# Kernel optimization log

Measured on AMD Instinct MI355X. Metric: run time of the kernel, lower is better.

The kernel has to match this reference:

```python
import jax, jax.numpy as jnp
import numpy as np

N_NODES = 100000
N_EDGES = 3200000
D_FEAT = 512
D_HID = 64
D_LAT = 16
N_CLASS = 10
N_FLOW = 10
K_PROP = 10
ALPHA_TELEPORT = 0.1


def setup_inputs() -> dict:
    key = jax.random.key(0)
    ks = jax.random.split(key, 8)
    x = jax.random.normal(ks[0], (N_NODES, D_FEAT), jnp.float32)
    edge_index = jax.random.randint(ks[1], (2, N_EDGES), 0, N_NODES)
    p_c = jax.random.uniform(ks[2], (N_CLASS,), jnp.float32) + 0.1
    p_c = p_c / p_c.sum()
    W1 = jax.random.normal(ks[3], (D_FEAT, D_HID), jnp.float32) / np.sqrt(D_FEAT).astype(np.float32)
    b1 = jnp.zeros((D_HID,), jnp.float32)
    W2 = jax.random.normal(ks[4], (D_HID, D_LAT), jnp.float32) / np.sqrt(D_HID).astype(np.float32)
    b2 = jnp.zeros((D_LAT,), jnp.float32)
    flow_z0 = jax.random.normal(ks[5], (N_FLOW, N_CLASS, D_LAT), jnp.float32) * 0.1
    flow_alpha_prime = jax.random.normal(ks[6], (N_FLOW, N_CLASS, 1), jnp.float32) * 0.1
    flow_beta = jax.random.normal(ks[7], (N_FLOW, N_CLASS, 1), jnp.float32) * 0.1
    return dict(x=x, edge_index=edge_index, p_c=p_c, W1=W1, b1=b1, W2=W2, b2=b2,
                flow_z0=flow_z0, flow_alpha_prime=flow_alpha_prime, flow_beta=flow_beta)


def _batched_radial_log_prob(z, flow_z0, flow_alpha_prime, flow_beta):
    # Per-class batched radial flow (invertible pyro-style parameterization).
    # z: [N, D] -> log_q: [N, C]
    C, D = flow_z0.shape[1], flow_z0.shape[2]
    zz = jnp.broadcast_to(z[None], (C, z.shape[0], D))  # [C, N, D]
    sum_logdet = jnp.zeros((C, z.shape[0]), z.dtype)
    for l in range(flow_z0.shape[0]):  # small fixed number of flow layers
        z0 = flow_z0[l][:, None, :]                               # [C,1,D]
        alpha = jax.nn.softplus(flow_alpha_prime[l])[:, None, :]  # [C,1,1]
        beta_hat = -alpha + jax.nn.softplus(flow_beta[l])[:, None, :]
        dz = zz - z0
        r = jnp.sqrt(jnp.sum(dz * dz, axis=-1, keepdims=True))    # [C,N,1]
        h = 1.0 / (alpha + r)
        bh = beta_hat * h
        zz = zz + bh * dz
        logdet = (D - 1) * jnp.log1p(bh) + jnp.log1p(bh - beta_hat * r * h * h)
        sum_logdet = sum_logdet + logdet[..., 0]
    log_base = -0.5 * jnp.sum(zz * zz, axis=-1) - 0.5 * D * jnp.log(2.0 * jnp.pi)
    return (log_base + sum_logdet).T  # [N, C]


def _appnp(beta_ft, edge_index, n_nodes):
    # APPNP with self loops and symmetric gcn normalization over edge list.
    src = jnp.concatenate([edge_index[0], jnp.arange(n_nodes)])
    dst = jnp.concatenate([edge_index[1], jnp.arange(n_nodes)])
    deg = jax.ops.segment_sum(jnp.ones_like(src, dtype=beta_ft.dtype), dst, num_segments=n_nodes)
    dinv = jnp.where(deg > 0, jax.lax.rsqrt(jnp.maximum(deg, 1.0)), 0.0)
    norm = (dinv[src] * dinv[dst])[:, None]  # [E+N, 1]
    x0 = beta_ft
    b = beta_ft
    for _ in range(K_PROP):
        agg = jax.ops.segment_sum(norm * b[src], dst, num_segments=n_nodes)
        b = (1.0 - ALPHA_TELEPORT) * agg + ALPHA_TELEPORT * x0
    return b


def reference(x, edge_index, p_c, W1, b1, W2, b2, flow_z0, flow_alpha_prime, flow_beta):
    h = jax.nn.relu(x @ W1 + b1)           # input_encoder (dropout inactive at eval)
    z = h @ W2 + b2                        # latent_encoder, [N, D_LAT]
    log_q = _batched_radial_log_prob(z, flow_z0, flow_alpha_prime, flow_beta)
    log_q_per_class = log_q + jnp.log(p_c)[None, :]
    log_scale = 0.5 * D_LAT * jnp.log(4.0 * jnp.pi)  # 'latent-new' evidence scale
    beta_ft = jnp.exp(jnp.clip(log_q_per_class + log_scale, -30.0, 30.0))
    beta = _appnp(beta_ft, edge_index, x.shape[0])
    alpha = 1.0 + beta
    soft = alpha / jnp.sum(alpha, axis=-1, keepdims=True)
    hard = jnp.argmax(soft, axis=-1)
    return hard[:, None], soft
```

## Files before the change

kernel.cpp:

```cpp
#include <hip/hip_runtime.h>
#include <math.h>
#include <limits.h>

#define DF 512
#define DH 64
#define DL 16
#define NC 10
#define NF 10
#define KPROP 10

#define BSH 7
#define BW  (1 << BSH)
#define MAXB 1024
#define TILE 16384

__device__ __forceinline__ float softplus_(float x){
  return fmaxf(x, 0.0f) + log1pf(expf(-fabsf(x)));
}

#define BM 64
#define BN 64
#define BK 32
__global__ __launch_bounds__(256) void k_gemm1z(const float* __restrict__ x,
    const float* __restrict__ W1, const float* __restrict__ b1,
    const float* __restrict__ W2, const float* __restrict__ b2,
    float* __restrict__ z, int N)
{
  __shared__ float smem[2*BK*(BM+4)];
  float (*At)[BM+4] = (float(*)[BM+4])smem;
  float (*Bs)[BN+4] = (float(*)[BN+4])(smem + BK*(BM+4));
  __shared__ float W2s[DH][DL];
  __shared__ float b2s[DL];
  const int tid = threadIdx.x;
  for (int i = tid; i < DH*DL; i += 256) W2s[i>>4][i&15] = W2[i];
  if (tid < DL) b2s[tid] = b2[tid];
  const int tx = tid & 15, ty = tid >> 4;
  const int row0 = blockIdx.x * BM;
  float acc[4][4] = {};
  for (int k0 = 0; k0 < DF; k0 += BK) {
    #pragma unroll
    for (int i = 0; i < 2; ++i) {
      int idx = tid + i*256;
      int r  = idx >> 3;
      int kk = (idx & 7) << 2;
      int row = row0 + r;
      float4 va = make_float4(0.f,0.f,0.f,0.f);
      if (row < N) va = *(const float4*)&x[(size_t)row*DF + k0 + kk];
      At[kk+0][r]=va.x; At[kk+1][r]=va.y; At[kk+2][r]=va.z; At[kk+3][r]=va.w;
      int r2 = idx >> 4;
      int c4 = (idx & 15) << 2;
      float4 vb = *(const float4*)&W1[(size_t)(k0+r2)*DH + c4];
      Bs[r2][c4+0]=vb.x; Bs[r2][c4+1]=vb.y; Bs[r2][c4+2]=vb.z; Bs[r2][c4+3]=vb.w;
    }
    __syncthreads();
    #pragma unroll
    for (int kk = 0; kk < BK; ++kk) {
      float4 av = *(const float4*)&At[kk][ty<<2];
      float4 bv = *(const float4*)&Bs[kk][tx<<2];
      float a4[4]={av.x,av.y,av.z,av.w};
      float b4[4]={bv.x,bv.y,bv.z,bv.w};
      #pragma unroll
      for (int i=0;i<4;++i)
        #pragma unroll
        for (int j=0;j<4;++j) acc[i][j] = fmaf(a4[i], b4[j], acc[i][j]);
    }
    __syncthreads();
  }
  float4 bias = ((const float4*)b1)[tx];
  float bias4[4] = {bias.x, bias.y, bias.z, bias.w};
  float (*hs)[BM+4] = (float(*)[BM+4])smem;
  #pragma unroll
  for (int i=0;i<4;++i){
    #pragma unroll
    for (int j=0;j<4;++j)
      hs[(ty<<2)+i][(tx<<2)+j] = fmaxf(acc[i][j] + bias4[j], 0.0f);
  }
  __syncthreads();
  int row = tid >> 2, lg = tid & 3;
  float4 zacc = ((const float4*)b2s)[lg];
  #pragma unroll 8
  for (int k = 0; k < DH; ++k){
    float hv = hs[row][k];
    float4 wv = *(const float4*)&W2s[k][lg<<2];
    zacc.x = fmaf(hv, wv.x, zacc.x);
    zacc.y = fmaf(hv, wv.y, zacc.y);
    zacc.z = fmaf(hv, wv.z, zacc.z);
    zacc.w = fmaf(hv, wv.w, zacc.w);
  }
  int grow = row0 + row;
  if (grow < N) ((float4*)z)[(size_t)grow*4 + lg] = zacc;
}

__global__ __launch_bounds__(256) void k_flow2(const float* __restrict__ z,
    const float* __restrict__ pc, const float* __restrict__ z0g,
    const float* __restrict__ apg, const float* __restrict__ fbg,
    const float* __restrict__ dinv,
    float* __restrict__ x0, float* __restrict__ c0, float* __restrict__ y0, int N)
{
  __shared__ float z0s[NF][NC][DL];
  __shared__ float alps[NF][NC];
  __shared__ float bhs[NF][NC];
  __shared__ float lpc[NC];
  int tid = threadIdx.x;
  for (int i = tid; i < NF*NC*DL; i += 256)
    z0s[(i>>4)/NC][(i>>4)%NC][i&15] = z0g[i];
  if (tid < NF*NC){
    int l = tid/NC, c = tid%NC;
    float al = softplus_(apg[tid]);
    alps[l][c] = al;
    bhs[l][c]  = -al + softplus_(fbg[tid]);
  }
  if (tid < NC) lpc[tid] = __logf(pc[tid]);
  __syncthreads();

  int idx = blockIdx.x*256 + tid;
  int n = idx >> 4, c = idx & 15;
  if (n >= N) return;
  float dn = dinv[n];
  if (c >= NC){ x0[idx] = 0.f; c0[idx] = 0.f; y0[idx] = 0.f; return; }

  float zz[DL];
  const float4* z4 = (const float4*)z;
  #pragma unroll
  for (int q=0; q<4; ++q){
    float4 v = z4[(size_t)n*4 + q];
    zz[q*4+0]=v.x; zz[q*4+1]=v.y; zz[q*4+2]=v.z; zz[q*4+3]=v.w;
  }
  const float NEGHALFD_LOG2PI = -14.703016531274762f;
  const float LOGSCALE        =  20.248193975754326f;
  float sld = 0.f;
  #pragma unroll 1
  for (int l=0; l<NF; ++l){
    float al = alps[l][c], bhat = bhs[l][c];
    float dz[DL]; float r2 = 0.f;
    #pragma unroll
    for (int d=0; d<DL; ++d){ float t = zz[d] - z0s[l][c][d]; dz[d]=t; r2 = fmaf(t,t,r2); }
    float r  = sqrtf(r2);
    float hh = 1.0f/(al + r);
    float bh = bhat*hh;
    #pragma unroll
    for (int d=0; d<DL; ++d) zz[d] = fmaf(bh, dz[d], zz[d]);
    sld += 15.0f*__logf(1.0f + bh) + __logf(1.0f + bh - bhat*r*hh*hh);
  }
  float q2 = 0.f;
  #pragma unroll
  for (int d=0; d<DL; ++d) q2 = fmaf(zz[d], zz[d], q2);
  float v = -0.5f*q2 + NEGHALFD_LOG2PI + sld + lpc[c] + LOGSCALE;
  v = fminf(fmaxf(v, -30.f), 30.f);
  float xv = __expf(v);
  x0[idx] = xv;
  c0[idx] = dn*xv;
  y0[idx] = 0.1f*dn*xv;
}

__global__ __launch_bounds__(256) void k_bhist(const int* __restrict__ dst,
    int* __restrict__ bCnt, int E, int B)
{
  __shared__ int hh[MAXB];
  int tid = threadIdx.x;
  for (int b = tid; b < B; b += 256) hh[b] = 0;
  __syncthreads();
  for (int i = blockIdx.x*256 + tid; i < E; i += gridDim.x*256)
    atomicAdd(&hh[dst[i] >> BSH], 1);
  __syncthreads();
  for (int b = tid; b < B; b += 256) if (hh[b]) atomicAdd(&bCnt[b], hh[b]);
}

__global__ __launch_bounds__(256) void k_scan_small(const int* __restrict__ in,
    int* __restrict__ out, int n, int writeTotal)
{
  __shared__ int sd[1024];
  int tid = threadIdx.x;
  int orig[4];
  #pragma unroll
  for (int j = 0; j < 4; ++j){
    int i = tid + j*256;
    orig[j] = (i < n) ? in[i] : 0;
    sd[i] = orig[j];
  }
  __syncthreads();
  for (int ofs = 1; ofs < 1024; ofs <<= 1){
    int vals[4];
    #pragma unroll
    for (int j = 0; j < 4; ++j){
      int i = tid + j*256;
      vals[j] = (i >= ofs) ? sd[i-ofs] : 0;
    }
    __syncthreads();
    #pragma unroll
    for (int j = 0; j < 4; ++j) sd[tid + j*256] += vals[j];
    __syncthreads();
  }
  #pragma unroll
  for (int j = 0; j < 4; ++j){
    int i = tid + j*256;
    if (i < n) out[i] = sd[i] - orig[j];
  }
  if (writeTotal && tid == 0) out[n] = sd[n-1];
}

__global__ __launch_bounds__(256) void k_bscatter(const int* __restrict__ src,
    const int* __restrict__ dst, const int* __restrict__ bOff,
    int* __restrict__ bCur, int* __restrict__ bp, int E, int B)
{
  __shared__ int hc[MAXB];
  __shared__ int hb[MAXB];
  int tid = threadIdx.x;
  int base = blockIdx.x * TILE;
  int lim  = base + TILE; if (lim > E) lim = E;
  for (int b = tid; b < B; b += 256) hc[b] = 0;
  __syncthreads();
  for (int i = base + tid; i < lim; i += 256)
    atomicAdd(&hc[dst[i] >> BSH], 1);
  __syncthreads();
  for (int b = tid; b < B; b += 256){
    int c = hc[b];
    hb[b] = c ? atomicAdd(&bCur[b], c) : 0;
    hc[b] = 0;
  }
  __syncthreads();
  for (int i = base + tid; i < lim; i += 256){
    int d = dst[i];
    int b = d >> BSH;
    int pos = bOff[b] + hb[b] + atomicAdd(&hc[b], 1);
    bp[pos] = (src[i] << BSH) | (d & (BW-1));
  }
}

__global__ __launch_bounds__(256) void k_bdeg(const int* __restrict__ bp,
    const int* __restrict__ bOff, int* __restrict__ deg,
    float* __restrict__ dinv, float* __restrict__ dinv2, int N)
{
  __shared__ int cur[BW];
  int tid = threadIdx.x;
  int b = blockIdx.x;
  if (tid < BW) cur[tid] = 0;
  __syncthreads();
  int s = bOff[b], e = bOff[b+1];
  for (int i = s + tid; i < e; i += 256)
    atomicAdd(&cur[bp[i] & (BW-1)], 1);
  __syncthreads();
  int node = (b << BSH) + tid;
  if (tid < BW && node < N){
    int d = cur[tid] + 1;
    deg[node] = d;
    float dv = 1.0f / sqrtf((float)d);
    dinv[node]  = dv;
    dinv2[node] = dv*dv;
  }
}

__global__ __launch_bounds__(256) void k_scan_part(const int* __restrict__ deg,
    int* __restrict__ part, int N){
  __shared__ int sd[256];
  int base = blockIdx.x*1024;
  int tid = threadIdx.x;
  int s = 0;
  #pragma unroll
  for (int i=0;i<4;++i){ int idx = base + tid*4 + i; if (idx < N) s += deg[idx]; }
  sd[tid] = s; __syncthreads();
  for (int ofs=128; ofs>0; ofs>>=1){ if (tid<ofs) sd[tid]+=sd[tid+ofs]; __syncthreads(); }
  if (tid==0) part[blockIdx.x] = sd[0];
}

__global__ __launch_bounds__(256) void k_scan_final(const int* __restrict__ deg,
    const int* __restrict__ part, int* __restrict__ off, int N, int E)
{
  __shared__ int sc[256];
  int base = blockIdx.x*1024;
  int tid = threadIdx.x;
  int v[4]; int s = 0;
  #pragma unroll
  for (int i=0;i<4;++i){ int idx = base + tid*4 + i; v[i] = (idx<N)?deg[idx]:0; s += v[i]; }
  sc[tid] = s; __syncthreads();
  for (int ofs=1; ofs<256; ofs<<=1){
    int t = (tid>=ofs) ? sc[tid-ofs] : 0;
    __syncthreads();
    sc[tid] += t;
    __syncthreads();
  }
  int ex = sc[tid] - s + part[blockIdx.x];
  #pragma unroll
  for (int i=0;i<4;++i){
    int idx = base + tid*4 + i;
    if (idx < N){
      off[idx] = ex;
      if (idx == N-1) off[N] = ex + v[i];
      ex += v[i];
    }
  }
}

__global__ __launch_bounds__(256) void k_place(const int* __restrict__ bp,
    const int* __restrict__ bOff, const int* __restrict__ off,
    int* __restrict__ csr, int N)
{
  __shared__ int cur[BW];
  int tid = threadIdx.x;
  int b = blockIdx.x;
  int node0 = b << BSH;
  if (tid < BW){
    cur[tid] = 1;
    int node = node0 + tid;
    if (node < N) csr[off[node]] = node;
  }
  __syncthreads();
  int s = bOff[b], e = bOff[b+1];
  for (int i = s + tid; i < e; i += 256){
    int v  = bp[i];
    int dl = v & (BW-1);
    int sn = v >> BSH;
    int d  = node0 + dl;
    int p  = off[d] + atomicAdd(&cur[dl], 1);
    csr[p] = sn;
  }
}

__global__ __launch_bounds__(256) void k_rank(int* __restrict__ csr,
    const int* __restrict__ off, int N)
{
  int wid  = (blockIdx.x*256 + threadIdx.x) >> 6;
  int lane = threadIdx.x & 63;
  if (wid >= N) return;
  int s = off[wid], e = off[wid+1];
  int d = e - s;
  if (d <= 1) return;
  if (d <= 64){
    int v = (lane < d) ? csr[s+lane] : INT_MAX;
    int rank = 0;
    for (int j = 0; j < d; ++j){
      int bv = __shfl(v, j);
      rank += (bv < v) || (bv == v && j < lane);
    }
    if (lane < d) csr[s+rank] = v;
  } else if (d <= 256){
    int v0 = (lane      < d) ? csr[s+lane      ] : INT_MAX;
    int v1 = (lane+64   < d) ? csr[s+lane+64   ] : INT_MAX;
    int v2 = (lane+128  < d) ? csr[s+lane+128  ] : INT_MAX;
    int v3 = (lane+192  < d) ? csr[s+lane+192  ] : INT_MAX;
    int r0=0,r1=0,r2=0,r3=0;
    for (int j = 0; j < d; ++j){
      int slot = j >> 6, jl = j & 63;
      int bv = (slot==0) ? __shfl(v0,jl) : (slot==1) ? __shfl(v1,jl)
             : (slot==2) ? __shfl(v2,jl) : __shfl(v3,jl);
      r0 += (bv < v0) || (bv == v0 && j < lane);
      r1 += (bv < v1) || (bv == v1 && j < lane+64);
      r2 += (bv < v2) || (bv == v2 && j < lane+128);
      r3 += (bv < v3) || (bv == v3 && j < lane+192);
    }
    if (lane      < d) csr[s+r0]=v0;
    if (lane+64   < d) csr[s+r1]=v1;
    if (lane+128  < d) csr[s+r2]=v2;
    if (lane+192  < d) csr[s+r3]=v3;
  } else {
    if (lane == 0){
      for (int i = s+1; i < e; ++i){
        int key = csr[i]; int j = i-1;
        while (j >= s && csr[j] > key){ csr[j+1] = csr[j]; --j; }
        csr[j+1] = key;
      }
    }
  }
}

__global__ __launch_bounds__(256) void k_prop(const float* __restrict__ cin,
    const float* __restrict__ y0, const float* __restrict__ dinv2,
    float* __restrict__ cout,
    const int* __restrict__ csr, const int* __restrict__ off, int N)
{
  int t = blockIdx.x*256 + threadIdx.x;
  int n = t / 12, sub = t - n*12;
  int q = sub >> 2, part = sub & 3;
  if (n >= N) return;
  const float4* c4 = (const float4*)cin;
  int s = off[n], e = off[n+1], d = e - s;
  int lo = s + ((d*part) >> 2);
  int hi = s + ((d*(part+1)) >> 2);
  float4 a0 = make_float4(0.f,0.f,0.f,0.f);
  float4 a1 = make_float4(0.f,0.f,0.f,0.f);
  int i = lo;
  for (; i+4 <= hi; i += 4){
    int s0=csr[i], s1=csr[i+1], s2=csr[i+2], s3=csr[i+3];
    float4 v0 = c4[(size_t)s0*4 + q];
    float4 v1 = c4[(size_t)s1*4 + q];
    float4 v2 = c4[(size_t)s2*4 + q];
    float4 v3 = c4[(size_t)s3*4 + q];
    a0.x+=v0.x; a0.y+=v0.y; a0.z+=v0.z; a0.w+=v0.w;
    a1.x+=v1.x; a1.y+=v1.y; a1.z+=v1.z; a1.w+=v1.w;
    a0.x+=v2.x; a0.y+=v2.y; a0.z+=v2.z; a0.w+=v2.w;
    a1.x+=v3.x; a1.y+=v3.y; a1.z+=v3.z; a1.w+=v3.w;
  }
  for (; i < hi; ++i){
    float4 v = c4[(size_t)csr[i]*4 + q];
    a0.x+=v.x; a0.y+=v.y; a0.z+=v.z; a0.w+=v.w;
  }
  float ax = a0.x+a1.x, ay = a0.y+a1.y, az = a0.z+a1.z, aw = a0.w+a1.w;
  ax += __shfl_xor(ax, 1, 4);  ay += __shfl_xor(ay, 1, 4);
  az += __shfl_xor(az, 1, 4);  aw += __shfl_xor(aw, 1, 4);
  ax += __shfl_xor(ax, 2, 4);  ay += __shfl_xor(ay, 2, 4);
  az += __shfl_xor(az, 2, 4);  aw += __shfl_xor(aw, 2, 4);
  if (part == 0){
    float w9 = 0.9f * dinv2[n];
    float4 yv = ((const float4*)y0)[(size_t)n*4 + q];
    float4 o;
    o.x = fmaf(w9, ax, yv.x);
    o.y = fmaf(w9, ay, yv.y);
    o.z = fmaf(w9, az, yv.z);
    o.w = fmaf(w9, aw, yv.w);
    ((float4*)cout)[(size_t)n*4 + q] = o;
  }
}

__global__ __launch_bounds__(256) void k_prop_final(const float* __restrict__ cin,
    const float* __restrict__ x0, const float* __restrict__ dinv,
    const int* __restrict__ csr, const int* __restrict__ off,
    float* __restrict__ out, int N)
{
  int t = blockIdx.x*256 + threadIdx.x;
  int n = t >> 4, sub = t & 15, q = sub & 3, part = sub >> 2;
  if (n >= N) return;
  const float4* c4 = (const float4*)cin;
  int s = off[n], e = off[n+1], d = e - s;
  int lo = s + ((d*part) >> 2);
  int hi = s + ((d*(part+1)) >> 2);
  float4 a0 = make_float4(0.f,0.f,0.f,0.f);
  float4 a1 = make_float4(0.f,0.f,0.f,0.f);
  if (q < 3){
    int i = lo;
    for (; i+4 <= hi; i += 4){
      int s0=csr[i], s1=csr[i+1], s2=csr[i+2], s3=csr[i+3];
      float4 v0 = c4[(size_t)s0*4 + q];
      float4 v1 = c4[(size_t)s1*4 + q];
      float4 v2 = c4[(size_t)s2*4 + q];
      float4 v3 = c4[(size_t)s3*4 + q];
      a0.x+=v0.x; a0.y+=v0.y; a0.z+=v0.z; a0.w+=v0.w;
      a1.x+=v1.x; a1.y+=v1.y; a1.z+=v1.z; a1.w+=v1.w;
      a0.x+=v2.x; a0.y+=v2.y; a0.z+=v2.z; a0.w+=v2.w;
      a1.x+=v3.x; a1.y+=v3.y; a1.z+=v3.z; a1.w+=v3.w;
    }
    for (; i < hi; ++i){
      float4 v = c4[(size_t)csr[i]*4 + q];
      a0.x+=v.x; a0.y+=v.y; a0.z+=v.z; a0.w+=v.w;
    }
  }
  float ax = a0.x+a1.x, ay = a0.y+a1.y, az = a0.z+a1.z, aw = a0.w+a1.w;
  ax += __shfl_xor(ax, 4, 16);  ay += __shfl_xor(ay, 4, 16);
  az += __shfl_xor(az, 4, 16);  aw += __shfl_xor(aw, 4, 16);
  ax += __shfl_xor(ax, 8, 16);  ay += __shfl_xor(ay, 8, 16);
  az += __shfl_xor(az, 8, 16);  aw += __shfl_xor(aw, 8, 16);
  if (part != 0) return;

  float w9 = 0.9f * dinv[n];
  float4 xv = ((const float4*)x0)[(size_t)n*4 + q];
  float4 al;
  al.x = fmaf(w9, ax, fmaf(0.1f, xv.x, 1.f));
  al.y = fmaf(w9, ay, fmaf(0.1f, xv.y, 1.f));
  al.z = fmaf(w9, az, fmaf(0.1f, xv.z, 1.f));
  al.w = fmaf(w9, aw, fmaf(0.1f, xv.w, 1.f));

  float sv = 0.f;
  if (q < 2)       sv = al.x + al.y + al.z + al.w;
  else if (q == 2) sv = al.x + al.y;
  sv += __shfl_xor(sv, 1, 4);
  sv += __shfl_xor(sv, 2, 4);

  float bv = -1e30f; int bi = 999;
  int cb = q*4;
  int nvalid = (q < 2) ? 4 : (q == 2 ? 2 : 0);
  float av[4] = {al.x, al.y, al.z, al.w};
  for (int j = 0; j < nvalid; ++j){
    if (av[j] > bv){ bv = av[j]; bi = cb + j; }
  }
  #pragma unroll
  for (int o = 1; o <= 2; o <<= 1){
    float vo = __shfl_xor(bv, o, 4);
    int  io  = __shfl_xor(bi, o, 4);
    if (vo > bv || (vo == bv && io < bi)){ bv = vo; bi = io; }
  }

  float inv = 1.0f / sv;
  size_t sb = (size_t)N + (size_t)n*NC;
  for (int j = 0; j < nvalid; ++j) out[sb + cb + j] = av[j] * inv;
  if (q == 0) out[n] = (float)bi;
}

extern "C" void kernel_launch(void* const* d_in, const int* in_sizes, int n_in,
                              void* d_out, int out_size, void* d_ws, size_t ws_size,
                              hipStream_t stream)
{
  const float* x  = (const float*)d_in[0];
  const int*   ei = (const int*)  d_in[1];
  const float* pc = (const float*)d_in[2];
  const float* W1 = (const float*)d_in[3];
  const float* b1 = (const float*)d_in[4];
  const float* W2 = (const float*)d_in[5];
  const float* b2 = (const float*)d_in[6];
  const float* z0 = (const float*)d_in[7];
  const float* ap = (const float*)d_in[8];
  const float* fb = (const float*)d_in[9];
  float* out = (float*)d_out;

  const int N = in_sizes[0] / DF;
  const int E = in_sizes[1] / 2;
  const int* src = ei;
  const int* dst = ei + E;
  const int B = (N + BW - 1) >> BSH;

  char* ws = (char*)d_ws;
  size_t o = 0;
  size_t region0 = (size_t)E*sizeof(int);
  if ((size_t)N*DL*sizeof(float) > region0) region0 = (size_t)N*DL*sizeof(float);
  int*   bp   = (int*)  (ws + o);
  float* z    = (float*)(ws + o);
  o += region0;
  int*   csr  = (int*)  (ws + o); o += (size_t)(E+N)*sizeof(int);
  float* x0   = (float*)(ws + o); o += (size_t)N*DL*sizeof(float);
  float* c0   = (float*)(ws + o); o += (size_t)N*DL*sizeof(float);
  float* y0   = (float*)(ws + o); o += (size_t)N*DL*sizeof(float);
  float* cA   = (float*)(ws + o); o += (size_t)N*DL*sizeof(float);
  float* cB   = (float*)(ws + o); o += (size_t)N*DL*sizeof(float);
  int*   deg  = (int*)  (ws + o); o += (size_t)N*sizeof(int);
  float* dinv = (float*)(ws + o); o += (size_t)N*sizeof(float);
  float* dinv2= (float*)(ws + o); o += (size_t)N*sizeof(float);
  int*   offs = (int*)  (ws + o); o += (size_t)(N+2)*sizeof(int);
  int*   part = (int*)  (ws + o); o += 4096;
  int*   bCnt = (int*)  (ws + o); o += MAXB*sizeof(int);
  int*   bOff = (int*)  (ws + o); o += (MAXB+1)*sizeof(int);
  int*   bCur = (int*)  (ws + o); o += MAXB*sizeof(int);

  const int TB = 256;
  int nb  = (N + 1023) / 1024;

  hipMemsetAsync(bCnt, 0, MAXB*sizeof(int), stream);
  hipMemsetAsync(bCur, 0, MAXB*sizeof(int), stream);
  k_bhist<<<512, TB, 0, stream>>>(dst, bCnt, E, B);
  k_scan_small<<<1, TB, 0, stream>>>(bCnt, bOff, B, 1);
  k_bscatter<<<(E + TILE - 1)/TILE, TB, 0, stream>>>(src, dst, bOff, bCur, bp, E, B);
  k_bdeg<<<B, TB, 0, stream>>>(bp, bOff, deg, dinv, dinv2, N);
  k_scan_part<<<nb, TB, 0, stream>>>(deg, part, N);
  k_scan_small<<<1, TB, 0, stream>>>(part, part, nb, 0);
  k_scan_final<<<nb, TB, 0, stream>>>(deg, part, offs, N, E);
  k_place<<<B, TB, 0, stream>>>(bp, bOff, offs, csr, N);
  k_rank<<<(N + 3) / 4, TB, 0, stream>>>(csr, offs, N);

  k_gemm1z<<<(N + BM - 1) / BM, TB, 0, stream>>>(x, W1, b1, W2, b2, z, N);
  k_flow2<<<((N*DL) + TB - 1) / TB, TB, 0, stream>>>(z, pc, z0, ap, fb, dinv,
                                                     x0, c0, y0, N);

  int gP = ((N*12) + TB - 1) / TB;
  const float* cin = c0;
  for (int it = 0; it < KPROP-1; ++it){
    float* cout = (it & 1) ? cB : cA;
    k_prop<<<gP, TB, 0, stream>>>(cin, y0, dinv2, cout, csr, offs, N);
    cin = cout;
  }
  int gF = ((N*16) + TB - 1) / TB;
  k_prop_final<<<gF, TB, 0, stream>>>(cin, x0, dinv, csr, offs, out, N);
}
```

Before: 741.8 us.

## Store propagation state in bf16 to halve gather traffic in APPNP iterations

The per-node propagated vectors used in the 10 APPNP gather iterations are stored as packed bf16 (16 bytes per 8 classes) instead of fp32, with fp32 accumulation. Each propagation kernel now uses 8 threads per node instead of 12 or 16 and unpacks bf16 pairs with shifts and masks. This cuts the random-gather bytes per edge, the main cost of the bandwidth-bound sparse aggregation. The trade-off is bf16 rounding of the intermediate state on every iteration, which may hurt accuracy and could change argmax ties.

Measured after the change: 647.2 us (median of 3 runs). -12.8%, faster.

```diff
diff --git a/kernel.cpp b/kernel.cpp
--- a/kernel.cpp
+++ b/kernel.cpp
@@ -16,6 +16,14 @@
 
 __device__ __forceinline__ float softplus_(float x){
   return fmaxf(x, 0.0f) + log1pf(expf(-fabsf(x)));
+}
+
+__device__ __forceinline__ unsigned int f2bf_(float f){
+  unsigned int u = __float_as_uint(f);
+  return (u + 0x7FFFu + ((u >> 16) & 1u)) >> 16;
+}
+__device__ __forceinline__ unsigned int pack2bf_(float lo, float hi){
+  return f2bf_(lo) | (f2bf_(hi) << 16);
 }
 
 #define BM 64
@@ -95,7 +103,8 @@
     const float* __restrict__ pc, const float* __restrict__ z0g,
     const float* __restrict__ apg, const float* __restrict__ fbg,
     const float* __restrict__ dinv,
-    float* __restrict__ x0, float* __restrict__ c0, float* __restrict__ y0, int N)
+    float* __restrict__ x0, unsigned short* __restrict__ c0b,
+    float* __restrict__ y0, int N)
 {
   __shared__ float z0s[NF][NC][DL];
   __shared__ float alps[NF][NC];
@@ -117,7 +126,7 @@
   int n = idx >> 4, c = idx & 15;
   if (n >= N) return;
   float dn = dinv[n];
-  if (c >= NC){ x0[idx] = 0.f; c0[idx] = 0.f; y0[idx] = 0.f; return; }
+  if (c >= NC){ x0[idx] = 0.f; c0b[idx] = 0; y0[idx] = 0.f; return; }
 
   float zz[DL];
   const float4* z4 = (const float4*)z;
@@ -149,8 +158,9 @@
   v = fminf(fmaxf(v, -30.f), 30.f);
   float xv = __expf(v);
   x0[idx] = xv;
-  c0[idx] = dn*xv;
-  y0[idx] = 0.1f*dn*xv;
+  float cv = dn*xv;
+  c0b[idx] = (unsigned short)f2bf_(cv);
+  y0[idx]  = 0.1f*cv;
 }
 
 __global__ __launch_bounds__(256) void k_bhist(const int* __restrict__ dst,
@@ -363,125 +373,136 @@
   }
 }
 
-__global__ __launch_bounds__(256) void k_prop(const float* __restrict__ cin,
+__global__ __launch_bounds__(256) void k_prop(const uint4* __restrict__ cin,
     const float* __restrict__ y0, const float* __restrict__ dinv2,
-    float* __restrict__ cout,
+    uint4* __restrict__ cout,
     const int* __restrict__ csr, const int* __restrict__ off, int N)
 {
   int t = blockIdx.x*256 + threadIdx.x;
-  int n = t / 12, sub = t - n*12;
-  int q = sub >> 2, part = sub & 3;
+  int n = t >> 3, sub = t & 7, qh = sub >> 2, part = sub & 3;
   if (n >= N) return;
-  const float4* c4 = (const float4*)cin;
   int s = off[n], e = off[n+1], d = e - s;
   int lo = s + ((d*part) >> 2);
   int hi = s + ((d*(part+1)) >> 2);
-  float4 a0 = make_float4(0.f,0.f,0.f,0.f);
-  float4 a1 = make_float4(0.f,0.f,0.f,0.f);
+  float a[8] = {0.f,0.f,0.f,0.f,0.f,0.f,0.f,0.f};
+  float b[8] = {0.f,0.f,0.f,0.f,0.f,0.f,0.f,0.f};
   int i = lo;
-  for (; i+4 <= hi; i += 4){
-    int s0=csr[i], s1=csr[i+1], s2=csr[i+2], s3=csr[i+3];
-    float4 v0 = c4[(size_t)s0*4 + q];
-    float4 v1 = c4[(size_t)s1*4 + q];
-    float4 v2 = c4[(size_t)s2*4 + q];
-    float4 v3 = c4[(size_t)s3*4 + q];
-    a0.x+=v0.x; a0.y+=v0.y; a0.z+=v0.z; a0.w+=v0.w;
-    a1.x+=v1.x; a1.y+=v1.y; a1.z+=v1.z; a1.w+=v1.w;
-    a0.x+=v2.x; a0.y+=v2.y; a0.z+=v2.z; a0.w+=v2.w;
-    a1.x+=v3.x; a1.y+=v3.y; a1.z+=v3.z; a1.w+=v3.w;
-  }
-  for (; i < hi; ++i){
-    float4 v = c4[(size_t)csr[i]*4 + q];
-    a0.x+=v.x; a0.y+=v.y; a0.z+=v.z; a0.w+=v.w;
-  }
-  float ax = a0.x+a1.x, ay = a0.y+a1.y, az = a0.z+a1.z, aw = a0.w+a1.w;
-  ax += __shfl_xor(ax, 1, 4);  ay += __shfl_xor(ay, 1, 4);
-  az += __shfl_xor(az, 1, 4);  aw += __shfl_xor(aw, 1, 4);
-  ax += __shfl_xor(ax, 2, 4);  ay += __shfl_xor(ay, 2, 4);
-  az += __shfl_xor(az, 2, 4);  aw += __shfl_xor(aw, 2, 4);
+  for (; i+2 <= hi; i += 2){
+    int s0 = csr[i], s1 = csr[i+1];
+    uint4 u0 = cin[(size_t)s0*2 + qh];
+    uint4 u1 = cin[(size_t)s1*2 + qh];
+    a[0] += __uint_as_float(u0.x << 16); a[1] += __uint_as_float(u0.x & 0xFFFF0000u);
+    a[2] += __uint_as_float(u0.y << 16); a[3] += __uint_as_float(u0.y & 0xFFFF0000u);
+    a[4] += __uint_as_float(u0.z << 16); a[5] += __uint_as_float(u0.z & 0xFFFF0000u);
+    a[6] += __uint_as_float(u0.w << 16); a[7] += __uint_as_float(u0.w & 0xFFFF0000u);
+    b[0] += __uint_as_float(u1.x << 16); b[1] += __uint_as_float(u1.x & 0xFFFF0000u);
+    b[2] += __uint_as_float(u1.y << 16); b[3] += __uint_as_float(u1.y & 0xFFFF0000u);
+    b[4] += __uint_as_float(u1.z << 16); b[5] += __uint_as_float(u1.z & 0xFFFF0000u);
+    b[6] += __uint_as_float(u1.w << 16); b[7] += __uint_as_float(u1.w & 0xFFFF0000u);
+  }
+  if (i < hi){
+    uint4 u0 = cin[(size_t)csr[i]*2 + qh];
+    a[0] += __uint_as_float(u0.x << 16); a[1] += __uint_as_float(u0.x & 0xFFFF0000u);
+    a[2] += __uint_as_float(u0.y << 16); a[3] += __uint_as_float(u0.y & 0xFFFF0000u);
+    a[4] += __uint_as_float(u0.z << 16); a[5] += __uint_as_float(u0.z & 0xFFFF0000u);
+    a[6] += __uint_as_float(u0.w << 16); a[7] += __uint_as_float(u0.w & 0xFFFF0000u);
+  }
+  float v[8];
+  #pragma unroll
+  for (int j = 0; j < 8; ++j){
+    float t2 = a[j] + b[j];
+    t2 += __shfl_xor(t2, 1, 4);
+    t2 += __shfl_xor(t2, 2, 4);
+    v[j] = t2;
+  }
   if (part == 0){
     float w9 = 0.9f * dinv2[n];
-    float4 yv = ((const float4*)y0)[(size_t)n*4 + q];
-    float4 o;
-    o.x = fmaf(w9, ax, yv.x);
-    o.y = fmaf(w9, ay, yv.y);
-    o.z = fmaf(w9, az, yv.z);
-    o.w = fmaf(w9, aw, yv.w);
-    ((float4*)cout)[(size_t)n*4 + q] = o;
-  }
-}
-
-__global__ __launch_bounds__(256) void k_prop_final(const float* __restrict__ cin,
+    const float4* y4 = (const float4*)y0;
+    float4 ya = y4[(size_t)n*4 + qh*2];
+    float4 yb = y4[(size_t)n*4 + qh*2 + 1];
+    float o0 = fmaf(w9, v[0], ya.x), o1 = fmaf(w9, v[1], ya.y);
+    float o2 = fmaf(w9, v[2], ya.z), o3 = fmaf(w9, v[3], ya.w);
+    float o4 = fmaf(w9, v[4], yb.x), o5 = fmaf(w9, v[5], yb.y);
+    float o6 = fmaf(w9, v[6], yb.z), o7 = fmaf(w9, v[7], yb.w);
+    uint4 w;
+    w.x = pack2bf_(o0, o1); w.y = pack2bf_(o2, o3);
+    w.z = pack2bf_(o4, o5); w.w = pack2bf_(o6, o7);
+    cout[(size_t)n*2 + qh] = w;
+  }
+}
+
+__global__ __launch_bounds__(256) void k_prop_final(const uint4* __restrict__ cin,
     const float* __restrict__ x0, const float* __restrict__ dinv,
     const int* __restrict__ csr, const int* __restrict__ off,
     float* __restrict__ out, int N)
 {
   int t = blockIdx.x*256 + threadIdx.x;
-  int n = t >> 4, sub = t & 15, q = sub & 3, part = sub >> 2;
+  int n = t >> 3, sub = t & 7, qh = sub >> 2, part = sub & 3;
   if (n >= N) return;
-  const float4* c4 = (const float4*)cin;
   int s = off[n], e = off[n+1], d = e - s;
   int lo = s + ((d*part) >> 2);
   int hi = s + ((d*(part+1)) >> 2);
-  float4 a0 = make_float4(0.f,0.f,0.f,0.f);
-  float4 a1 = make_float4(0.f,0.f,0.f,0.f);
-  if (q < 3){
-    int i = lo;
-    for (; i+4 <= hi; i += 4){
-      int s0=csr[i], s1=csr[i+1], s2=csr[i+2], s3=csr[i+3];
-      float4 v0 = c4[(size_t)s0*4 + q];
-      float4 v1 = c4[(size_t)s1*4 + q];
-      float4 v2 = c4[(size_t)s2*4 + q];
-      float4 v3 = c4[(size_t)s3*4 + q];
-      a0.x+=v0.x; a0.y+=v0.y; a0.z+=v0.z; a0.w+=v0.w;
-      a1.x+=v1.x; a1.y+=v1.y; a1.z+=v1.z; a1.w+=v1.w;
-      a0.x+=v2.x; a0.y+=v2.y; a0.z+=v2.z; a0.w+=v2.w;
-      a1.x+=v3.x; a1.y+=v3.y; a1.z+=v3.z; a1.w+=v3.w;
-    }
-    for (; i < hi; ++i){
-      float4 v = c4[(size_t)csr[i]*4 + q];
-      a0.x+=v.x; a0.y+=v.y; a0.z+=v.z; a0.w+=v.w;
-    }
-  }
-  float ax = a0.x+a1.x, ay = a0.y+a1.y, az = a0.z+a1.z, aw = a0.w+a1.w;
-  ax += __shfl_xor(ax, 4, 16);  ay += __shfl_xor(ay, 4, 16);
-  az += __shfl_xor(az, 4, 16);  aw += __shfl_xor(aw, 4, 16);
-  ax += __shfl_xor(ax, 8, 16);  ay += __shfl_xor(ay, 8, 16);
-  az += __shfl_xor(az, 8, 16);  aw += __shfl_xor(aw, 8, 16);
+  float a[8] = {0.f,0.f,0.f,0.f,0.f,0.f,0.f,0.f};
+  float b[8] = {0.f,0.f,0.f,0.f,0.f,0.f,0.f,0.f};
+  int i = lo;
+  for (; i+2 <= hi; i += 2){
+    int s0 = csr[i], s1 = csr[i+1];
+    uint4 u0 = cin[(size_t)s0*2 + qh];
+    uint4 u1 = cin[(size_t)s1*2 + qh];
+    a[0] += __uint_as_float(u0.x << 16); a[1] += __uint_as_float(u0.x & 0xFFFF0000u);
+    a[2] += __uint_as_float(u0.y << 16); a[3] += __uint_as_float(u0.y & 0xFFFF0000u);
+    a[4] += __uint_as_float(u0.z << 16); a[5] += __uint_as_float(u0.z & 0xFFFF0000u);
+    a[6] += __uint_as_float(u0.w << 16); a[7] += __uint_as_float(u0.w & 0xFFFF0000u);
+    b[0] += __uint_as_float(u1.x << 16); b[1] += __uint_as_float(u1.x & 0xFFFF0000u);
+    b[2] += __uint_as_float(u1.y << 16); b[3] += __uint_as_float(u1.y & 0xFFFF0000u);
+    b[4] += __uint_as_float(u1.z << 16); b[5] += __uint_as_float(u1.z & 0xFFFF0000u);
+    b[6] += __uint_as_float(u1.w << 16); b[7] += __uint_as_float(u1.w & 0xFFFF0000u);
+  }
+  if (i < hi){
+    uint4 u0 = cin[(size_t)csr[i]*2 + qh];
+    a[0] += __uint_as_float(u0.x << 16); a[1] += __uint_as_float(u0.x & 0xFFFF0000u);
+    a[2] += __uint_as_float(u0.y << 16); a[3] += __uint_as_float(u0.y & 0xFFFF0000u);
+    a[4] += __uint_as_float(u0.z << 16); a[5] += __uint_as_float(u0.z & 0xFFFF0000u);
+    a[6] += __uint_as_float(u0.w << 16); a[7] += __uint_as_float(u0.w & 0xFFFF0000u);
+  }
+  float v[8];
+  #pragma unroll
+  for (int j = 0; j < 8; ++j){
+    float t2 = a[j] + b[j];
+    t2 += __shfl_xor(t2, 1, 4);
+    t2 += __shfl_xor(t2, 2, 4);
+    v[j] = t2;
+  }
   if (part != 0) return;
 
   float w9 = 0.9f * dinv[n];
-  float4 xv = ((const float4*)x0)[(size_t)n*4 + q];
-  float4 al;
-  al.x = fmaf(w9, ax, fmaf(0.1f, xv.x, 1.f));
-  al.y = fmaf(w9, ay, fmaf(0.1f, xv.y, 1.f));
-  al.z = fmaf(w9, az, fmaf(0.1f, xv.z, 1.f));
-  al.w = fmaf(w9, aw, fmaf(0.1f, xv.w, 1.f));
-
+  const float4* x4 = (const float4*)x0;
+  float4 xa = x4[(size_t)n*4 + qh*2];
+  float4 xb = x4[(size_t)n*4 + qh*2 + 1];
+  float xv[8] = {xa.x, xa.y, xa.z, xa.w, xb.x, xb.y, xb.z, xb.w};
+  float al[8];
+  #pragma unroll
+  for (int j = 0; j < 8; ++j) al[j] = fmaf(w9, v[j], fmaf(0.1f, xv[j], 1.f));
+
+  int nv = qh ? 2 : 8;
   float sv = 0.f;
-  if (q < 2)       sv = al.x + al.y + al.z + al.w;
-  else if (q == 2) sv = al.x + al.y;
-  sv += __shfl_xor(sv, 1, 4);
-  sv += __shfl_xor(sv, 2, 4);
+  for (int j = 0; j < nv; ++j) sv += al[j];
+  sv += __shfl_xor(sv, 4, 8);
 
   float bv = -1e30f; int bi = 999;
-  int cb = q*4;
-  int nvalid = (q < 2) ? 4 : (q == 2 ? 2 : 0);
-  float av[4] = {al.x, al.y, al.z, al.w};
-  for (int j = 0; j < nvalid; ++j){
-    if (av[j] > bv){ bv = av[j]; bi = cb + j; }
-  }
-  #pragma unroll
-  for (int o = 1; o <= 2; o <<= 1){
-    float vo = __shfl_xor(bv, o, 4);
-    int  io  = __shfl_xor(bi, o, 4);
+  for (int j = 0; j < nv; ++j){
+    if (al[j] > bv){ bv = al[j]; bi = qh*8 + j; }
+  }
+  {
+    float vo = __shfl_xor(bv, 4, 8);
+    int  io  = __shfl_xor(bi, 4, 8);
     if (vo > bv || (vo == bv && io < bi)){ bv = vo; bi = io; }
   }
 
   float inv = 1.0f / sv;
   size_t sb = (size_t)N + (size_t)n*NC;
-  for (int j = 0; j < nvalid; ++j) out[sb + cb + j] = av[j] * inv;
-  if (q == 0) out[n] = (float)bi;
+  for (int j = 0; j < nv; ++j) out[sb + qh*8 + j] = al[j] * inv;
+  if (sub == 0) out[n] = (float)bi;
 }
 
 extern "C" void kernel_launch(void* const* d_in, const int* in_sizes, int n_in,
@@ -515,10 +536,10 @@
   o += region0;
   int*   csr  = (int*)  (ws + o); o += (size_t)(E+N)*sizeof(int);
   float* x0   = (float*)(ws + o); o += (size_t)N*DL*sizeof(float);
-  float* c0   = (float*)(ws + o); o += (size_t)N*DL*sizeof(float);
   float* y0   = (float*)(ws + o); o += (size_t)N*DL*sizeof(float);
-  float* cA   = (float*)(ws + o); o += (size_t)N*DL*sizeof(float);
-  float* cB   = (float*)(ws + o); o += (size_t)N*DL*sizeof(float);
+  unsigned short* c0b = (unsigned short*)(ws + o); o += (size_t)N*DL*2;
+  unsigned short* cAb = (unsigned short*)(ws + o); o += (size_t)N*DL*2;
+  unsigned short* cBb = (unsigned short*)(ws + o); o += (size_t)N*DL*2;
   int*   deg  = (int*)  (ws + o); o += (size_t)N*sizeof(int);
   float* dinv = (float*)(ws + o); o += (size_t)N*sizeof(float);
   float* dinv2= (float*)(ws + o); o += (size_t)N*sizeof(float);
@@ -545,15 +566,16 @@
 
   k_gemm1z<<<(N + BM - 1) / BM, TB, 0, stream>>>(x, W1, b1, W2, b2, z, N);
   k_flow2<<<((N*DL) + TB - 1) / TB, TB, 0, stream>>>(z, pc, z0, ap, fb, dinv,
-                                                     x0, c0, y0, N);
-
-  int gP = ((N*12) + TB - 1) / TB;
-  const float* cin = c0;
+                                                     x0, c0b, y0, N);
+
+  int gP = ((N*8) + TB - 1) / TB;
+  const unsigned short* cin = c0b;
   for (int it = 0; it < KPROP-1; ++it){
-    float* cout = (it & 1) ? cB : cA;
-    k_prop<<<gP, TB, 0, stream>>>(cin, y0, dinv2, cout, csr, offs, N);
+    unsigned short* cout = (it & 1) ? cBb : cAb;
+    k_prop<<<gP, TB, 0, stream>>>((const uint4*)cin, y0, dinv2,
+                                  (uint4*)cout, csr, offs, N);
     cin = cout;
   }
-  int gF = ((N*16) + TB - 1) / TB;
-  k_prop_final<<<gF, TB, 0, stream>>>(cin, x0, dinv, csr, offs, out, N);
-}
+  k_prop_final<<<gP, TB, 0, stream>>>((const uint4*)cin, x0, dinv,
+                                      csr, offs, out, N);
+}
```
